# Kernel optimization log

Hardware: AMD Instinct MI355X
Metric: run time of the kernel (lower is better)

## Reference

```python
import jax, jax.numpy as jnp
import numpy as np

B, T, D_MODEL, N_HEADS = 2, 2048, 1024, 16
HEAD_DIM = D_MODEL // N_HEADS          # 64
CODE_SIZE = HEAD_DIM // 4              # 16


def setup_inputs() -> dict:
    key = jax.random.key(0)
    k1, k2, k3, k4 = jax.random.split(key, 4)
    x = jax.random.normal(k1, (B, T, D_MODEL), dtype=jnp.float32)
    # nn.Linear weights (out_features, in_features), fan-in init scale
    w_qkv = jax.random.normal(k2, (3 * D_MODEL, D_MODEL), dtype=jnp.float32) / np.sqrt(D_MODEL)
    w_out = jax.random.normal(k3, (D_MODEL, D_MODEL), dtype=jnp.float32) / np.sqrt(D_MODEL)
    fc_code = jax.random.normal(k4, (1, N_HEADS, CODE_SIZE, HEAD_DIM), dtype=jnp.float32)
    return {"x": x, "w_qkv": w_qkv, "w_out": w_out, "fc_code": fc_code}


def reference(x, w_qkv, w_out, fc_code):
    Bx, Tx, _ = x.shape
    scale = HEAD_DIM ** (-0.5)
    qkv = x @ w_qkv.T                                   # (B,T,3*d_model)
    # split_heads with Hs=head_dim on 3*d_model -> (B, 3*nH, T, Hs), then chunk on head axis
    qkv = qkv.reshape(Bx, Tx, 3 * N_HEADS, HEAD_DIM).transpose(0, 2, 1, 3)
    q, k, v = qkv[:, :N_HEADS], qkv[:, N_HEADS:2 * N_HEADS], qkv[:, 2 * N_HEADS:]
    code = fc_code[0]                                   # (nH, C, Hs)
    q = jnp.einsum('bhtd,hcd->bhtc', q, code) * scale   # (B,H,T,C)
    k = jnp.einsum('bhtd,hcd->bhtc', k, code) * scale
    q = jax.nn.softmax(q, axis=-1) * scale
    # causal branch (mask is None)
    k_exp = jnp.exp(k - jnp.max(k, axis=2, keepdims=True))       # (B,H,T,C)
    k_exp_cumsum = jnp.cumsum(k_exp, axis=2)                      # (B,H,T,C)
    kv_cumsum = jnp.cumsum(jnp.einsum('bhtc,bhtd->bhtcd', k_exp, v), axis=2)  # (B,H,T,C,D)
    kv = kv_cumsum / (k_exp_cumsum[..., None] + 1e-9)
    xo = jnp.einsum('bhtc,bhtcd->bhtd', q, kv)                    # (B,H,T,D)
    xo = xo.transpose(0, 2, 1, 3).reshape(Bx, Tx, D_MODEL)        # cat_heads
    return xo @ w_out.T
```

## Files before the change

kernel.cpp:

```cpp
#include <hip/hip_runtime.h>
#include <math.h>

#define B_    2
#define T_    2048
#define D_    1024
#define H_    16
#define HD_   64
#define C_    16
#define SCALE_ 0.125f
#define L_    128
#define NC_   16
#define NW_   1536

typedef __attribute__((ext_vector_type(8))) short short8;
typedef __attribute__((ext_vector_type(4))) float f32x4;

__device__ inline float b2f(uint32_t u16) {
    return __uint_as_float(u16 << 16);
}
__device__ inline ushort f2b(float f) {
    uint32_t u = __float_as_uint(f);
    return (ushort)((u + 0x7FFFu + ((u >> 16) & 1u)) >> 16);
}
__device__ inline uint32_t pack2(float a, float b) {
    return (uint32_t)f2b(a) | ((uint32_t)f2b(b) << 16);
}
__device__ inline void unpack2(uint32_t w, float& a, float& b) {
    a = b2f(w & 0xffffu); b = __uint_as_float(w & 0xffff0000u);
}
__device__ inline void unpack8(uint4 raw, float* dst) {
    unpack2(raw.x, dst[0], dst[1]);
    unpack2(raw.y, dst[2], dst[3]);
    unpack2(raw.z, dst[4], dst[5]);
    unpack2(raw.w, dst[6], dst[7]);
}
__device__ __forceinline__ void gll16(const ushort* g, ushort* l) {
    __builtin_amdgcn_global_load_lds(
        (const __attribute__((address_space(1))) void*)g,
        (__attribute__((address_space(3))) void*)l, 16, 0, 0);
}

__global__ __launch_bounds__(256)
void cast_bf16_kernel(const float* __restrict__ in, ushort* __restrict__ out, int n) {
    int i = (blockIdx.x * 256 + threadIdx.x) * 8;
    if (i >= n) return;
    float4 a = *(const float4*)(in + i);
    float4 b = *(const float4*)(in + i + 4);
    uint4 o;
    o.x = pack2(a.x, a.y); o.y = pack2(a.z, a.w);
    o.z = pack2(b.x, b.y); o.w = pack2(b.z, b.w);
    *(uint4*)(out + i) = o;
}

__global__ __launch_bounds__(256)
void cast_w2_kernel(const float* __restrict__ w_qkv, const float* __restrict__ w_out,
                    ushort* __restrict__ WallB, ushort* __restrict__ WoB) {
    const int bid = blockIdx.x;
    const int isW = bid >> 9;
    const float* in = isW ? w_out : (w_qkv + (size_t)2048 * 1024);
    ushort* out = isW ? WoB : (WallB + (size_t)512 * 1024);
    const int i = (bid & 511) * 2048 + threadIdx.x * 8;
    float4 a = *(const float4*)(in + i);
    float4 b = *(const float4*)(in + i + 4);
    uint4 o;
    o.x = pack2(a.x, a.y); o.y = pack2(a.z, a.w);
    o.z = pack2(b.x, b.y); o.w = pack2(b.z, b.w);
    *(uint4*)(out + i) = o;
}

__global__ __launch_bounds__(256)
void fold_code_kernel(const float* __restrict__ w_qkv, const float* __restrict__ code,
                      ushort* __restrict__ WallB) {
    const int bid = blockIdx.x;
    const int isK = bid >> 8;
    const int row = bid & 255;
    const int h = row >> 4;
    __shared__ float cs[HD_];
    if (threadIdx.x < HD_) cs[threadIdx.x] = code[row * HD_ + threadIdx.x];
    __syncthreads();
    const float* wbase = w_qkv + (size_t)(isK * D_ + h * HD_) * D_;
    ushort* outp = WallB + (size_t)(isK * 256 + row) * D_;
    for (int e = threadIdx.x; e < D_; e += 256) {
        float acc = 0.f;
        #pragma unroll 8
        for (int d = 0; d < HD_; ++d) acc += wbase[(size_t)d * D_ + e] * cs[d];
        outp[e] = f2b(acc * SCALE_);
    }
}

template<int WRITE_BF16>
__global__ __launch_bounds__(256)
void gemm_bf16_kernel(const ushort* __restrict__ A, const ushort* __restrict__ Bw,
                      void* __restrict__ Cv, int M, int N, int K) {
    __shared__ ushort As[2][128 * 64];
    __shared__ ushort Bs[2][128 * 64];
    const int tid  = threadIdx.x;
    const int wave = tid >> 6;
    const int lane = tid & 63;
    const int wr = wave >> 1, wc = wave & 1;

    const int gx = gridDim.x;
    int f = blockIdx.y * gx + blockIdx.x;
    const int nwg = gx * gridDim.y;
    if ((nwg & 7) == 0) f = (f & 7) * (nwg >> 3) + (f >> 3);
    const int row0 = (f / gx) * 128;
    const int col0 = (f % gx) * 128;

    f32x4 acc[4][4];
    #pragma unroll
    for (int m = 0; m < 4; ++m)
        #pragma unroll
        for (int n = 0; n < 4; ++n) acc[m][n] = (f32x4){0.f, 0.f, 0.f, 0.f};

    const int srow = lane >> 3;
    const int kA   = ((lane & 7) ^ srow) << 3;
    const int lane15 = lane & 15;
    const int lhi    = lane >> 4;
    const int axor   = (lane15 & 7) << 4;

    const int NT = K >> 6;

    #pragma unroll
    for (int i = 0; i < 4; ++i) {
        const int seg = wave * 4 + i;
        const int r = seg * 8 + srow;
        gll16(A  + (size_t)(row0 + r) * K + kA, &As[0][seg * 512]);
        gll16(Bw + (size_t)(col0 + r) * K + kA, &Bs[0][seg * 512]);
    }
    __syncthreads();

    for (int it = 0; it < NT; ++it) {
        const int cur = it & 1;
        if (it + 1 < NT) {
            const int kk = (it + 1) << 6;
            #pragma unroll
            for (int i = 0; i < 4; ++i) {
                const int seg = wave * 4 + i;
                const int r = seg * 8 + srow;
                gll16(A  + (size_t)(row0 + r) * K + kk + kA, &As[cur ^ 1][seg * 512]);
                gll16(Bw + (size_t)(col0 + r) * K + kk + kA, &Bs[cur ^ 1][seg * 512]);
            }
        }
        const char* Ab = (const char*)As[cur];
        const char* Bb = (const char*)Bs[cur];
        #pragma unroll
        for (int s = 0; s < 2; ++s) {
            short8 af[4], bf[4];
            #pragma unroll
            for (int m = 0; m < 4; ++m) {
                const int r = wr * 64 + m * 16 + lane15;
                const int off = (r * 128 + s * 64 + lhi * 16) ^ axor;
                af[m] = *(const short8*)(Ab + off);
            }
            #pragma unroll
            for (int n = 0; n < 4; ++n) {
                const int r = wc * 64 + n * 16 + lane15;
                const int off = (r * 128 + s * 64 + lhi * 16) ^ axor;
                bf[n] = *(const short8*)(Bb + off);
            }
            #pragma unroll
            for (int m = 0; m < 4; ++m)
                #pragma unroll
                for (int n = 0; n < 4; ++n)
                    acc[m][n] = __builtin_amdgcn_mfma_f32_16x16x32_bf16(
                        af[m], bf[n], acc[m][n], 0, 0, 0);
        }
        __syncthreads();
    }

    #pragma unroll
    for (int m = 0; m < 4; ++m) {
        #pragma unroll
        for (int n = 0; n < 4; ++n) {
            const int row = row0 + wr * 64 + m * 16 + lhi * 4;
            const int col = col0 + wc * 64 + n * 16 + lane15;
            if (WRITE_BF16) {
                ushort* C = (ushort*)Cv;
                #pragma unroll
                for (int j = 0; j < 4; ++j)
                    C[(size_t)(row + j) * N + col] = f2b(acc[m][n][j]);
            } else {
                float* C = (float*)Cv;
                #pragma unroll
                for (int j = 0; j < 4; ++j)
                    C[(size_t)(row + j) * N + col] = acc[m][n][j];
            }
        }
    }
}

__global__ __launch_bounds__(256)
void prep_attn_kernel(const ushort* __restrict__ qkcv, ushort* __restrict__ vT,
                      float* __restrict__ ke_loc, float* __restrict__ kv_loc) {
    const int bid = blockIdx.x;
    const int chunk = bid & (NC_ - 1);
    const int bh = bid >> 4;
    const int b = bh >> 4, h = bh & 15;
    const int t0 = chunk * L_;
    const int tid = threadIdx.x;
    __shared__ __align__(16) ushort tile[128 * 64];
    __shared__ float ke_s[L_][C_];
    __shared__ float gsum[C_][16];
    char* tB = (char*)tile;

    #pragma unroll
    for (int r = 0; r < 4; ++r) {
        const int idx = r * 2048 + tid * 8;
        const int t = idx >> 6, d0 = idx & 63;
        uint4 raw = *(const uint4*)(qkcv + (size_t)(b * T_ + t0 + t) * NW_ + 512 + h * 64 + d0);
        *(uint4*)(tB + ((t * 128 + d0 * 2) ^ (((t >> 3) & 7) << 4))) = raw;
    }
    {
        const int t = tid >> 1, c0 = (tid & 1) * 8;
        uint4 raw = *(const uint4*)(qkcv + (size_t)(b * T_ + t0 + t) * NW_ + 256 + h * C_ + c0);
        float f[8]; unpack8(raw, f);
        #pragma unroll
        for (int j = 0; j < 8; ++j) ke_s[t][c0 + j] = __expf(f[j]);
    }
    __syncthreads();

    {
        const int d = tid >> 2, tq = tid & 3;
        ushort* obase = vT + ((size_t)bh * 64 + d) * 2048 + t0;
        #pragma unroll
        for (int c8 = 0; c8 < 4; ++c8) {
            const int tA = c8 * 32 + tq * 8;
            uint32_t w[4];
            #pragma unroll
            for (int p = 0; p < 4; ++p) {
                const int tL = tA + p * 2;
                uint32_t lo = *(const ushort*)(tB + ((tL * 128 + d * 2) ^ (((tL >> 3) & 7) << 4)));
                uint32_t hi = *(const ushort*)(tB + (((tL + 1) * 128 + d * 2) ^ ((((tL + 1) >> 3) & 7) << 4)));
                w[p] = lo | (hi << 16);
            }
            uint4 o; o.x = w[0]; o.y = w[1]; o.z = w[2]; o.w = w[3];
            *(uint4*)(obase + tA) = o;
        }
    }

    const int c = tid >> 4;
    const int dg = (tid & 15) << 2;
    float a0 = 0.f, a1 = 0.f, a2 = 0.f, a3 = 0.f;
    for (int t = 0; t < L_; ++t) {
        const float kev = ke_s[t][c];
        uint2 rv = *(const uint2*)(tB + ((t * 128 + dg * 2) ^ (((t >> 3) & 7) << 4)));
        float v0, v1, v2, v3;
        unpack2(rv.x, v0, v1); unpack2(rv.y, v2, v3);
        a0 += kev * v0; a1 += kev * v1; a2 += kev * v2; a3 += kev * v3;
    }
    {
        const int cc = tid & 15, g = tid >> 4;
        float s = 0.f;
        #pragma unroll
        for (int u = 0; u < 8; ++u) s += ke_s[g * 8 + u][cc];
        gsum[cc][g] = s;
    }
    __syncthreads();
    if (tid < C_) {
        float s = 0.f;
        #pragma unroll
        for (int g = 0; g < 16; ++g) s += gsum[tid][g];
        ke_loc[(size_t)bid * C_ + tid] = s;
    }
    *(float4*)(kv_loc + (size_t)bid * 1024 + c * HD_ + dg) = make_float4(a0, a1, a2, a3);
}

__global__ __launch_bounds__(1024)
void chunk_scan_kernel(float* __restrict__ ke_loc, float* __restrict__ kv_loc) {
    const int bh = blockIdx.x;
    const int tid = threadIdx.x;
    float run = 0.f;
    for (int ch = 0; ch < NC_; ++ch) {
        size_t idx = ((size_t)(bh * NC_ + ch)) * 1024 + tid;
        float tmp = kv_loc[idx];
        kv_loc[idx] = run;
        run += tmp;
    }
    if (tid < C_) {
        float run2 = 0.f;
        for (int ch = 0; ch < NC_; ++ch) {
            size_t idx = ((size_t)(bh * NC_ + ch)) * C_ + tid;
            float tmp = ke_loc[idx];
            ke_loc[idx] = run2;
            run2 += tmp;
        }
    }
}

__global__ __launch_bounds__(256)
void intra_kernel(const ushort* __restrict__ qkcv, const ushort* __restrict__ vT,
                  const float* __restrict__ ke_loc, const float* __restrict__ kv_loc,
                  ushort* __restrict__ xob) {
    const int bid = blockIdx.x;
    const int chunk = bid & (NC_ - 1);
    const int bh = bid >> 4;
    const int b = bh >> 4, h = bh & 15;
    const int t0 = chunk * L_;
    const int tid = threadIdx.x;
    const int wave = tid >> 6, lane = tid & 63;
    const int l15 = lane & 15, lhi = lane >> 4;

    __shared__ __align__(16) ushort ke_bf[128 * 32];
    __shared__ __align__(16) ushort qn_bf[128 * 32];
    __shared__ __align__(16) ushort Vt_s[64 * 128];
    __shared__ __align__(16) ushort Pl[128 * 128];
    __shared__ __align__(16) ushort S0t[64 * 32];
    __shared__ float kesum_s[128][16];
    __shared__ float gsum[16][16];
    __shared__ float e0s[16];

    char* keB = (char*)ke_bf;
    char* qnB = (char*)qn_bf;
    char* vtB = (char*)Vt_s;
    char* plB = (char*)Pl;
    char* s0B = (char*)S0t;

    {
        const int t = tid >> 1, c0 = (tid & 1) * 8;
        uint4 raw = *(const uint4*)(qkcv + (size_t)(b * T_ + t0 + t) * NW_ + 256 + h * C_ + c0);
        float f[8]; unpack8(raw, f);
        uint4 o;
        o.x = pack2(__expf(f[0]), __expf(f[1]));
        o.y = pack2(__expf(f[2]), __expf(f[3]));
        o.z = pack2(__expf(f[4]), __expf(f[5]));
        o.w = pack2(__expf(f[6]), __expf(f[7]));
        const int swz = ((t >> 1) & 3) << 4;
        *(uint4*)(keB + ((t * 64 + c0 * 2) ^ swz)) = o;
        *(uint4*)(keB + ((t * 64 + 32 + c0 * 2) ^ swz)) = make_uint4(0, 0, 0, 0);
    }
    {
        const int d = tid >> 2, q = tid & 3;
        const ushort* src = vT + ((size_t)bh * 64 + d) * 2048 + t0 + q * 32;
        const int swz = (d & 15) << 4;
        #pragma unroll
        for (int i = 0; i < 4; ++i) {
            uint4 raw = *(const uint4*)(src + i * 8);
            *(uint4*)(vtB + ((d * 256 + q * 64 + i * 16) ^ swz)) = raw;
        }
    }
    {
        const int c = tid >> 4;
        const int d0 = (tid & 15) * 4;
        float4 s4 = *(const float4*)(kv_loc + (size_t)bid * 1024 + c * 64 + d0);
        const float* sp = (const float*)&s4;
        #pragma unroll
        for (int j = 0; j < 4; ++j) {
            const int d = d0 + j;
            const int swz2 = ((d >> 1) & 3) << 4;
            *(ushort*)(s0B + ((d * 64 + c * 2) ^ swz2)) = f2b(sp[j]);
        }
        const int dz = tid >> 2;
        const int off = 32 + (tid & 3) * 8;
        const int swzz = ((dz >> 1) & 3) << 4;
        *(uint2*)(s0B + ((dz * 64 + off) ^ swzz)) = make_uint2(0, 0);
    }
    if (tid < 16) e0s[tid] = ke_loc[(size_t)bid * C_ + tid];
    __syncthreads();

    {
        const int cc = tid & 15, g = tid >> 4;
        float s = 0.f;
        #pragma unroll
        for (int u = 0; u < 8; ++u) {
            const int t = g * 8 + u;
            s += b2f(*(const ushort*)(keB + ((t * 64 + cc * 2) ^ (((t >> 1) & 3) << 4))));
        }
        gsum[cc][g] = s;
    }
    __syncthreads();
    if (tid < 16) {
        float run = e0s[tid];
        #pragma unroll
        for (int g = 0; g < 16; ++g) { float tmp = gsum[tid][g]; gsum[tid][g] = run; run += tmp; }
    }
    __syncthreads();
    {
        const int cc = tid & 15, g = tid >> 4;
        float run = gsum[cc][g];
        #pragma unroll
        for (int u = 0; u < 8; ++u) {
            const int t = g * 8 + u;
            run += b2f(*(const ushort*)(keB + ((t * 64 + cc * 2) ^ (((t >> 1) & 3) << 4))));
            kesum_s[t][cc] = run;
        }
    }
    __syncthreads();

    if (tid < 128) {
        const int t = tid;
        const ushort* qrow = qkcv + (size_t)(b * T_ + t0 + t) * NW_ + h * C_;
        float qv[16];
        uint4 r0 = *(const uint4*)qrow, r1 = *(const uint4*)(qrow + 8);
        unpack8(r0, qv); unpack8(r1, qv + 8);
        float m = qv[0];
        #pragma unroll
        for (int c = 1; c < 16; ++c) m = fmaxf(m, qv[c]);
        float sum = 0.f;
        #pragma unroll
        for (int c = 0; c < 16; ++c) { qv[c] = __expf(qv[c] - m); sum += qv[c]; }
        const float inv = SCALE_ / sum;
        #pragma unroll
        for (int c = 0; c < 16; ++c) qv[c] = qv[c] * inv / (kesum_s[t][c] + 1e-9f);
        uint4 o0, o1;
        o0.x = pack2(qv[0], qv[1]);   o0.y = pack2(qv[2], qv[3]);
        o0.z = pack2(qv[4], qv[5]);   o0.w = pack2(qv[6], qv[7]);
        o1.x = pack2(qv[8], qv[9]);   o1.y = pack2(qv[10], qv[11]);
        o1.z = pack2(qv[12], qv[13]); o1.w = pack2(qv[14], qv[15]);
        const int swz = ((t >> 1) & 3) << 4;
        *(uint4*)(qnB + ((t * 64) ^ swz)) = o0;
        *(uint4*)(qnB + ((t * 64 + 16) ^ swz)) = o1;
        *(uint4*)(qnB + ((t * 64 + 32) ^ swz)) = make_uint4(0, 0, 0, 0);
        *(uint4*)(qnB + ((t * 64 + 48) ^ swz)) = make_uint4(0, 0, 0, 0);
    }
    __syncthreads();

    #pragma unroll
    for (int sr = 0; sr < 2; ++sr) {
        const int sb = wave * 2 + sr;
        const int s_row = sb * 16 + l15;
        short8 af = *(const short8*)(keB + ((s_row * 64 + lhi * 16) ^ (((s_row >> 1) & 3) << 4)));
        #pragma unroll
        for (int tb = 0; tb < 8; ++tb) {
            f32x4 p = (f32x4){0.f, 0.f, 0.f, 0.f};
            if (tb >= sb) {
                const int t_col = tb * 16 + l15;
                short8 bf = *(const short8*)(qnB + ((t_col * 64 + lhi * 16) ^ (((t_col >> 1) & 3) << 4)));
                p = __builtin_amdgcn_mfma_f32_16x16x32_bf16(af, bf, p, 0, 0, 0);
                if (tb == sb) {
                    #pragma unroll
                    for (int j = 0; j < 4; ++j)
                        p[j] = (lhi * 4 + j > l15) ? 0.f : p[j];
                }
            }
            const int t_g = tb * 16 + l15;
            const int sbase = sb * 16 + lhi * 4;
            const int swz = (t_g & 15) << 4;
            *(uint32_t*)(plB + ((t_g * 256 + sbase * 2) ^ swz)) = pack2(p[0], p[1]);
            *(uint32_t*)(plB + ((t_g * 256 + sbase * 2 + 4) ^ swz)) = pack2(p[2], p[3]);
        }
    }
    __syncthreads();

    f32x4 acc[2][4];
    #pragma unroll
    for (int tt = 0; tt < 2; ++tt)
        #pragma unroll
        for (int dt = 0; dt < 4; ++dt) acc[tt][dt] = (f32x4){0.f, 0.f, 0.f, 0.f};

    const int trow = wave * 32;
    #pragma unroll
    for (int tt = 0; tt < 2; ++tt) {
        const int t_g = trow + tt * 16 + l15;
        short8 aq = *(const short8*)(qnB + ((t_g * 64 + lhi * 16) ^ (((t_g >> 1) & 3) << 4)));
        #pragma unroll
        for (int dt = 0; dt < 4; ++dt) {
            const int d = dt * 16 + l15;
            short8 bs = *(const short8*)(s0B + ((d * 64 + lhi * 16) ^ (((d >> 1) & 3) << 4)));
            acc[tt][dt] = __builtin_amdgcn_mfma_f32_16x16x32_bf16(aq, bs, acc[tt][dt], 0, 0, 0);
        }
        const int pswz = (t_g & 15) << 4;
        #pragma unroll
        for (int kb = 0; kb < 4; ++kb) {
            short8 ap = *(const short8*)(plB + ((t_g * 256 + kb * 64 + lhi * 16) ^ pswz));
            #pragma unroll
            for (int dt = 0; dt < 4; ++dt) {
                const int d = dt * 16 + l15;
                short8 bv = *(const short8*)(vtB + ((d * 256 + kb * 64 + lhi * 16) ^ ((d & 15) << 4)));
                acc[tt][dt] = __builtin_amdgcn_mfma_f32_16x16x32_bf16(ap, bv, acc[tt][dt], 0, 0, 0);
            }
        }
    }

    #pragma unroll
    for (int tt = 0; tt < 2; ++tt) {
        const int tg0 = t0 + trow + tt * 16 + lhi * 4;
        #pragma unroll
        for (int dt = 0; dt < 4; ++dt) {
            const int d = dt * 16 + l15;
            ushort* orow = xob + (size_t)(b * T_ + tg0) * D_ + h * HD_ + d;
            #pragma unroll
            for (int j = 0; j < 4; ++j)
                orow[(size_t)j * D_] = f2b(acc[tt][dt][j]);
        }
    }
}

extern "C" void kernel_launch(void* const* d_in, const int* in_sizes, int n_in,
                              void* d_out, int out_size, void* d_ws, size_t ws_size,
                              hipStream_t stream) {
    const float* x     = (const float*)d_in[0];
    const float* w_qkv = (const float*)d_in[1];
    const float* w_out = (const float*)d_in[2];
    const float* code  = (const float*)d_in[3];
    float* out = (float*)d_out;

    ushort* xb    = (ushort*)d_ws;
    ushort* WallB = xb + (size_t)4096 * 1024;
    ushort* WoB   = WallB + (size_t)1536 * 1024;
    ushort* qkcv  = WoB + (size_t)1024 * 1024;
    ushort* xob   = qkcv + (size_t)4096 * 1536;
    ushort* vT    = xob + (size_t)4096 * 1024;
    float*  ke_loc = (float*)(vT + (size_t)32 * 64 * 2048);
    float*  kv_loc = ke_loc + 512 * 16;

    cast_bf16_kernel<<<2048, 256, 0, stream>>>(x, xb, 4096 * 1024);
    cast_w2_kernel<<<1024, 256, 0, stream>>>(w_qkv, w_out, WallB, WoB);
    fold_code_kernel<<<512, 256, 0, stream>>>(w_qkv, code, WallB);

    gemm_bf16_kernel<1><<<dim3(12, 32), 256, 0, stream>>>(xb, WallB, qkcv, 4096, NW_, 1024);

    prep_attn_kernel<<<512, 256, 0, stream>>>(qkcv, vT, ke_loc, kv_loc);
    chunk_scan_kernel<<<32, 1024, 0, stream>>>(ke_loc, kv_loc);
    intra_kernel<<<512, 256, 0, stream>>>(qkcv, vT, ke_loc, kv_loc, xob);

    gemm_bf16_kernel<0><<<dim3(8, 32), 256, 0, stream>>>(xob, WoB, out, 4096, 1024, 1024);
}
```

Before: 93.60 us.

## Merge input-prep kernels and fold chunk prefix scan into intra kernel

```diff
diff --git a/kernel.cpp b/kernel.cpp
--- a/kernel.cpp
+++ b/kernel.cpp
@@ -41,50 +41,47 @@
 }
 
 __global__ __launch_bounds__(256)
-void cast_bf16_kernel(const float* __restrict__ in, ushort* __restrict__ out, int n) {
-    int i = (blockIdx.x * 256 + threadIdx.x) * 8;
-    if (i >= n) return;
-    float4 a = *(const float4*)(in + i);
-    float4 b = *(const float4*)(in + i + 4);
-    uint4 o;
-    o.x = pack2(a.x, a.y); o.y = pack2(a.z, a.w);
-    o.z = pack2(b.x, b.y); o.w = pack2(b.z, b.w);
-    *(uint4*)(out + i) = o;
-}
-
-__global__ __launch_bounds__(256)
-void cast_w2_kernel(const float* __restrict__ w_qkv, const float* __restrict__ w_out,
-                    ushort* __restrict__ WallB, ushort* __restrict__ WoB) {
+void prep_inputs_kernel(const float* __restrict__ x, const float* __restrict__ w_qkv,
+                        const float* __restrict__ w_out, const float* __restrict__ code,
+                        ushort* __restrict__ xb, ushort* __restrict__ WallB,
+                        ushort* __restrict__ WoB) {
     const int bid = blockIdx.x;
-    const int isW = bid >> 9;
-    const float* in = isW ? w_out : (w_qkv + (size_t)2048 * 1024);
-    ushort* out = isW ? WoB : (WallB + (size_t)512 * 1024);
-    const int i = (bid & 511) * 2048 + threadIdx.x * 8;
-    float4 a = *(const float4*)(in + i);
-    float4 b = *(const float4*)(in + i + 4);
-    uint4 o;
-    o.x = pack2(a.x, a.y); o.y = pack2(a.z, a.w);
-    o.z = pack2(b.x, b.y); o.w = pack2(b.z, b.w);
-    *(uint4*)(out + i) = o;
-}
-
-__global__ __launch_bounds__(256)
-void fold_code_kernel(const float* __restrict__ w_qkv, const float* __restrict__ code,
-                      ushort* __restrict__ WallB) {
-    const int bid = blockIdx.x;
-    const int isK = bid >> 8;
-    const int row = bid & 255;
-    const int h = row >> 4;
-    __shared__ float cs[HD_];
-    if (threadIdx.x < HD_) cs[threadIdx.x] = code[row * HD_ + threadIdx.x];
-    __syncthreads();
-    const float* wbase = w_qkv + (size_t)(isK * D_ + h * HD_) * D_;
-    ushort* outp = WallB + (size_t)(isK * 256 + row) * D_;
-    for (int e = threadIdx.x; e < D_; e += 256) {
-        float acc = 0.f;
-        #pragma unroll 8
-        for (int d = 0; d < HD_; ++d) acc += wbase[(size_t)d * D_ + e] * cs[d];
-        outp[e] = f2b(acc * SCALE_);
+    if (bid < 3072) {
+        const float* in;
+        ushort* out;
+        int i;
+        if (bid < 2048) {
+            in = x; out = xb;
+            i = bid * 2048 + threadIdx.x * 8;
+        } else {
+            const int sub = bid - 2048;
+            const int isW = sub >> 9;
+            in = isW ? w_out : (w_qkv + (size_t)2048 * 1024);
+            out = isW ? WoB : (WallB + (size_t)512 * 1024);
+            i = (sub & 511) * 2048 + threadIdx.x * 8;
+        }
+        float4 a = *(const float4*)(in + i);
+        float4 b = *(const float4*)(in + i + 4);
+        uint4 o;
+        o.x = pack2(a.x, a.y); o.y = pack2(a.z, a.w);
+        o.z = pack2(b.x, b.y); o.w = pack2(b.z, b.w);
+        *(uint4*)(out + i) = o;
+    } else {
+        const int sub = bid - 3072;
+        const int isK = sub >> 8;
+        const int row = sub & 255;
+        const int h = row >> 4;
+        __shared__ float cs[HD_];
+        if (threadIdx.x < HD_) cs[threadIdx.x] = code[row * HD_ + threadIdx.x];
+        __syncthreads();
+        const float* wbase = w_qkv + (size_t)(isK * D_ + h * HD_) * D_;
+        ushort* outp = WallB + (size_t)(isK * 256 + row) * D_;
+        for (int e = threadIdx.x; e < D_; e += 256) {
+            float acc = 0.f;
+            #pragma unroll 8
+            for (int d = 0; d < HD_; ++d) acc += wbase[(size_t)d * D_ + e] * cs[d];
+            outp[e] = f2b(acc * SCALE_);
+        }
     }
 }
 
@@ -265,28 +262,6 @@
     *(float4*)(kv_loc + (size_t)bid * 1024 + c * HD_ + dg) = make_float4(a0, a1, a2, a3);
 }
 
-__global__ __launch_bounds__(1024)
-void chunk_scan_kernel(float* __restrict__ ke_loc, float* __restrict__ kv_loc) {
-    const int bh = blockIdx.x;
-    const int tid = threadIdx.x;
-    float run = 0.f;
-    for (int ch = 0; ch < NC_; ++ch) {
-        size_t idx = ((size_t)(bh * NC_ + ch)) * 1024 + tid;
-        float tmp = kv_loc[idx];
-        kv_loc[idx] = run;
-        run += tmp;
-    }
-    if (tid < C_) {
-        float run2 = 0.f;
-        for (int ch = 0; ch < NC_; ++ch) {
-            size_t idx = ((size_t)(bh * NC_ + ch)) * C_ + tid;
-            float tmp = ke_loc[idx];
-            ke_loc[idx] = run2;
-            run2 += tmp;
-        }
-    }
-}
-
 __global__ __launch_bounds__(256)
 void intra_kernel(const ushort* __restrict__ qkcv, const ushort* __restrict__ vT,
                   const float* __restrict__ ke_loc, const float* __restrict__ kv_loc,
@@ -341,8 +316,13 @@
     {
         const int c = tid >> 4;
         const int d0 = (tid & 15) * 4;
-        float4 s4 = *(const float4*)(kv_loc + (size_t)bid * 1024 + c * 64 + d0);
-        const float* sp = (const float*)&s4;
+        const float* base = kv_loc + (size_t)(bh * NC_) * 1024 + c * 64 + d0;
+        float s0 = 0.f, s1 = 0.f, s2 = 0.f, s3 = 0.f;
+        for (int ch = 0; ch < chunk; ++ch) {
+            float4 t4 = *(const float4*)(base + ch * 1024);
+            s0 += t4.x; s1 += t4.y; s2 += t4.z; s3 += t4.w;
+        }
+        const float sp[4] = {s0, s1, s2, s3};
         #pragma unroll
         for (int j = 0; j < 4; ++j) {
             const int d = d0 + j;
@@ -354,7 +334,12 @@
         const int swzz = ((dz >> 1) & 3) << 4;
         *(uint2*)(s0B + ((dz * 64 + off) ^ swzz)) = make_uint2(0, 0);
     }
-    if (tid < 16) e0s[tid] = ke_loc[(size_t)bid * C_ + tid];
+    if (tid < 16) {
+        float s = 0.f;
+        for (int ch = 0; ch < chunk; ++ch)
+            s += ke_loc[(size_t)(bh * NC_ + ch) * C_ + tid];
+        e0s[tid] = s;
+    }
     __syncthreads();
 
     {
@@ -503,14 +488,11 @@
     float*  ke_loc = (float*)(vT + (size_t)32 * 64 * 2048);
     float*  kv_loc = ke_loc + 512 * 16;
 
-    cast_bf16_kernel<<<2048, 256, 0, stream>>>(x, xb, 4096 * 1024);
-    cast_w2_kernel<<<1024, 256, 0, stream>>>(w_qkv, w_out, WallB, WoB);
-    fold_code_kernel<<<512, 256, 0, stream>>>(w_qkv, code, WallB);
+    prep_inputs_kernel<<<3584, 256, 0, stream>>>(x, w_qkv, w_out, code, xb, WallB, WoB);
 
     gemm_bf16_kernel<1><<<dim3(12, 32), 256, 0, stream>>>(xb, WallB, qkcv, 4096, NW_, 1024);
 
     prep_attn_kernel<<<512, 256, 0, stream>>>(qkcv, vT, ke_loc, kv_loc);
-    chunk_scan_kernel<<<32, 1024, 0, stream>>>(ke_loc, kv_loc);
     intra_kernel<<<512, 256, 0, stream>>>(qkcv, vT, ke_loc, kv_loc, xob);
 
     gemm_bf16_kernel<0><<<dim3(8, 32), 256, 0, stream>>>(xob, WoB, out, 4096, 1024, 1024);
```

Result: faster. 90.67 us (-3.1%).
